# Performance work log

Hardware: AMD Instinct MI355X
Metric: run time of the kernel (lower is better)

## Reference

```python
import jax, jax.numpy as jnp
import numpy as np


def setup_inputs() -> dict:
    key = jax.random.key(0)
    k0, k1, k2 = jax.random.split(key, 3)
    B, C, N, M = 2, 64, 1024, 32
    C_mid = 16  # bottleneck of the AFA weight-learning MLP (C -> C//4 -> C)
    feature = jax.random.normal(k0, (B, C, N, M), dtype=jnp.float32)
    W1 = (jax.random.normal(k1, (C_mid, C), dtype=jnp.float32) / np.float32(np.sqrt(C)))
    b1 = jnp.zeros((C_mid,), dtype=jnp.float32)
    W2 = (jax.random.normal(k2, (C, C_mid), dtype=jnp.float32) / np.float32(np.sqrt(C_mid)))
    b2 = jnp.zeros((C,), dtype=jnp.float32)
    return {"feature": feature, "W1": W1, "b1": b1, "W2": W2, "b2": b2}


def reference(feature, W1, b1, W2, b2):
    # feature: (B, C, N, M)
    B, C, N, M = feature.shape
    eye = jnp.eye(M, dtype=feature.dtype)  # (M, M)
    # pair[b,c,n,i,j] = f_i - f_j + f_i * delta_ij  (the repeat/transpose/eye trick)
    fi = feature[..., :, None]                      # (B, C, N, M, 1)
    pair = fi - feature[..., None, :] + fi * eye    # (B, C, N, M, M)
    # 1x1-conv MLP over channel dim (SharedMLP: C -> C_mid -> C), ReLU between
    h = jax.nn.relu(jnp.einsum('oc,bcnij->bonij', W1, pair)
                    + b1[None, :, None, None, None])
    w = (jnp.einsum('oc,bcnij->bonij', W2, h)
         + b2[None, :, None, None, None])           # (B, C, N, M, M)
    w = jax.nn.softmax(w, axis=-1)                  # use_softmax=True, over last dim
    # weighted-sum aggregation over j -> (B, C, N, M)
    return jnp.sum(pair * w, axis=-1)
```

## Files before the change

### kernel.cpp

```cpp
#include <hip/hip_runtime.h>
#include <stdint.h>

namespace {
constexpr int NM = 1024 * 32;

typedef _Float16 half8 __attribute__((ext_vector_type(8)));
typedef float floatx16 __attribute__((ext_vector_type(16)));

__global__ __launch_bounds__(256, 3) void afa_kernel(
    const float* __restrict__ feat,
    const float* __restrict__ W1,
    const float* __restrict__ b1,
    const float* __restrict__ W2,
    float* __restrict__ out)
{
  __shared__ __align__(16) float f_c[64 * 34];
  __shared__ __align__(16) float g1T[16 * 33];
  __shared__ __align__(16) float w1s[16 * 68];
  __shared__ __align__(16) float edia[64 * 34];
  __shared__ __align__(16) float outs[64 * 34];

  const int t = threadIdx.x;
  const int bn = blockIdx.x;
  const size_t base = (size_t)(bn >> 10) * (64 * NM) + (size_t)(bn & 1023) * 32;

  {
    const int o = t >> 4, cq = t & 15;
    reinterpret_cast<float4*>(w1s)[o * 17 + cq] =
        reinterpret_cast<const float4*>(W1)[t];
  }
  {
    const int m = t & 31, c0 = t >> 5;
    #pragma unroll
    for (int r = 0; r < 8; ++r) {
      const int c = c0 + 8 * r;
      f_c[c * 34 + m] = feat[base + (size_t)c * NM + m];
    }
  }
  __syncthreads();

  {
    const int m = t & 31;
    const int o2 = t >> 5;
    const float* wa = w1s + o2 * 68;
    const float* wb = w1s + (o2 + 8) * 68;
    float a0 = 0.f, a1 = 0.f;
    #pragma unroll
    for (int c = 0; c < 64; ++c) {
      const float v = f_c[c * 34 + m];
      a0 = fmaf(wa[c], v, a0);
      a1 = fmaf(wb[c], v, a1);
    }
    g1T[o2 * 33 + m] = a0;
    g1T[(o2 + 8) * 33 + m] = a1;
  }
  __syncthreads();

  const int w  = t >> 6;
  const int ln = t & 63;
  const int cl = ln & 31;
  const int hl = ln >> 5;

  half8 B0, B1;
  {
    const float4* w2a = reinterpret_cast<const float4*>(W2 + cl * 16 + 8 * hl);
    const float4 x = w2a[0], y = w2a[1];
    B0[0] = (_Float16)x.x; B0[1] = (_Float16)x.y; B0[2] = (_Float16)x.z; B0[3] = (_Float16)x.w;
    B0[4] = (_Float16)y.x; B0[5] = (_Float16)y.y; B0[6] = (_Float16)y.z; B0[7] = (_Float16)y.w;
    const float4* w2b = reinterpret_cast<const float4*>(W2 + (cl + 32) * 16 + 8 * hl);
    const float4 u = w2b[0], v = w2b[1];
    B1[0] = (_Float16)u.x; B1[1] = (_Float16)u.y; B1[2] = (_Float16)u.z; B1[3] = (_Float16)u.w;
    B1[4] = (_Float16)v.x; B1[5] = (_Float16)v.y; B1[6] = (_Float16)v.z; B1[7] = (_Float16)v.w;
  }
  float b1r[8];
  {
    const float4* bb = reinterpret_cast<const float4*>(b1 + 8 * hl);
    const float4 x = bb[0], y = bb[1];
    b1r[0] = x.x; b1r[1] = x.y; b1r[2] = x.z; b1r[3] = x.w;
    b1r[4] = y.x; b1r[5] = y.y; b1r[6] = y.z; b1r[7] = y.w;
  }
  float g1j[8];
  #pragma unroll
  for (int q = 0; q < 8; ++q) g1j[q] = g1T[(8 * hl + q) * 33 + cl];

  float fcol0[16], fcol1[16];
  #pragma unroll
  for (int r = 0; r < 16; ++r) {
    const int jr = (r & 3) + 8 * (r >> 2) + 4 * hl;
    fcol0[r] = f_c[cl * 34 + jr];
    fcol1[r] = f_c[(cl + 32) * 34 + jr];
  }

  if (w == 0) {
    half8 Ad;
    #pragma unroll
    for (int q = 0; q < 8; ++q) Ad[q] = (_Float16)fmaxf(g1j[q] + b1r[q], 0.f);
    floatx16 d0, d1;
    #pragma unroll
    for (int r = 0; r < 16; ++r) { d0[r] = 0.f; d1[r] = 0.f; }
    d0 = __builtin_amdgcn_mfma_f32_32x32x16_f16(Ad, B0, d0, 0, 0, 0);
    d1 = __builtin_amdgcn_mfma_f32_32x32x16_f16(Ad, B1, d1, 0, 0, 0);
    #pragma unroll
    for (int r = 0; r < 16; ++r) {
      const int ir = (r & 3) + 8 * (r >> 2) + 4 * hl;
      edia[cl * 34 + ir]        = __expf(d0[r]);
      edia[(cl + 32) * 34 + ir] = __expf(d1[r]);
    }
  }
  __syncthreads();

  #pragma unroll 2
  for (int ii = 0; ii < 8; ++ii) {
    const int i = w * 8 + ii;
    half8 A;
    const bool dg = (cl == i);
    #pragma unroll
    for (int q = 0; q < 8; ++q) {
      const float gp = g1T[(8 * hl + q) * 33 + i] + b1r[q];
      const float h = gp - (dg ? 0.f : g1j[q]);
      A[q] = (_Float16)fmaxf(h, 0.f);
    }
    floatx16 acc0, acc1;
    #pragma unroll
    for (int r = 0; r < 16; ++r) { acc0[r] = 0.f; acc1[r] = 0.f; }
    acc0 = __builtin_amdgcn_mfma_f32_32x32x16_f16(A, B0, acc0, 0, 0, 0);
    acc1 = __builtin_amdgcn_mfma_f32_32x32x16_f16(A, B1, acc1, 0, 0, 0);

    float Sa = 0.f, Sb = 0.f, Da = 0.f, Db = 0.f;
    float Sc = 0.f, Sd = 0.f, Dc = 0.f, Dd = 0.f;
    #pragma unroll
    for (int r = 0; r < 16; r += 2) {
      const float e0 = __expf(acc0[r]);
      const float e1 = __expf(acc0[r + 1]);
      Sa += e0; Sb += e1;
      Da = fmaf(fcol0[r], e0, Da);
      Db = fmaf(fcol0[r + 1], e1, Db);
      const float e2 = __expf(acc1[r]);
      const float e3 = __expf(acc1[r + 1]);
      Sc += e2; Sd += e3;
      Dc = fmaf(fcol1[r], e2, Dc);
      Dd = fmaf(fcol1[r + 1], e3, Dd);
    }
    float S0 = Sa + Sb, D0 = Da + Db;
    float S1 = Sc + Sd, D1 = Dc + Dd;
    S0 += __shfl_xor(S0, 32);
    D0 += __shfl_xor(D0, 32);
    S1 += __shfl_xor(S1, 32);
    D1 += __shfl_xor(D1, 32);

    const float fi0 = f_c[cl * 34 + i];
    const float ei0 = edia[cl * 34 + i];
    const float fi1 = f_c[(cl + 32) * 34 + i];
    const float ei1 = edia[(cl + 32) * 34 + i];
    const float inv0 = 1.0f / S0;
    const float inv1 = 1.0f / S1;
    outs[cl * 34 + i]        = fi0 * (1.0f + ei0 * inv0) - D0 * inv0;
    outs[(cl + 32) * 34 + i] = fi1 * (1.0f + ei1 * inv1) - D1 * inv1;
  }
  __syncthreads();

  {
    const int m = t & 31, c0 = t >> 5;
    #pragma unroll
    for (int r = 0; r < 8; ++r) {
      const int cc = c0 + 8 * r;
      out[base + (size_t)cc * NM + m] = outs[cc * 34 + m];
    }
  }
}
}

extern "C" void kernel_launch(void* const* d_in, const int* in_sizes, int n_in,
                              void* d_out, int out_size, void* d_ws, size_t ws_size,
                              hipStream_t stream) {
  const float* feat = (const float*)d_in[0];
  const float* W1   = (const float*)d_in[1];
  const float* b1   = (const float*)d_in[2];
  const float* W2   = (const float*)d_in[3];
  float* out = (float*)d_out;

  afa_kernel<<<dim3(2 * 1024), dim3(256), 0, stream>>>(feat, W1, b1, W2, out);
}
```

Baseline: 38.85 us.

## Fold log2e into W2, use exp2 and packed math, cut LDS and raise occupancy

Pre-scales W2 by log2(e) so the softmax exponentials become native exp2 calls. The first-layer bias is folded into the g1 accumulation, and g1 is stored row-major so each i row can be read with float4 loads. fp16 conversion uses packed cvt_pkrtz, and the S/D reductions use 2-wide vectors. The output buffer is aliased onto edia, which removes one LDS array and lets launch bounds target 6 blocks per CU. The risks are register spills under the tighter bound and small numeric changes from round-toward-zero conversion.

```diff
diff --git a/kernel.cpp b/kernel.cpp
--- a/kernel.cpp
+++ b/kernel.cpp
@@ -3,11 +3,20 @@
 
 namespace {
 constexpr int NM = 1024 * 32;
+constexpr float LOG2E = 1.44269504088896340736f;
 
 typedef _Float16 half8 __attribute__((ext_vector_type(8)));
 typedef float floatx16 __attribute__((ext_vector_type(16)));
-
-__global__ __launch_bounds__(256, 3) void afa_kernel(
+typedef float f2v __attribute__((ext_vector_type(2)));
+
+__device__ __forceinline__ uint32_t pkrtz_bits(float a, float b) {
+  auto pk = __builtin_amdgcn_cvt_pkrtz(a, b);
+  uint32_t u;
+  __builtin_memcpy(&u, &pk, 4);
+  return u;
+}
+
+__global__ __launch_bounds__(256, 6) void afa_kernel(
     const float* __restrict__ feat,
     const float* __restrict__ W1,
     const float* __restrict__ b1,
@@ -15,15 +24,44 @@
     float* __restrict__ out)
 {
   __shared__ __align__(16) float f_c[64 * 34];
-  __shared__ __align__(16) float g1T[16 * 33];
+  __shared__ __align__(16) float g1b[32 * 20];
   __shared__ __align__(16) float w1s[16 * 68];
   __shared__ __align__(16) float edia[64 * 34];
-  __shared__ __align__(16) float outs[64 * 34];
 
   const int t = threadIdx.x;
   const int bn = blockIdx.x;
   const size_t base = (size_t)(bn >> 10) * (64 * NM) + (size_t)(bn & 1023) * 32;
 
+  const int w  = t >> 6;
+  const int ln = t & 63;
+  const int cl = ln & 31;
+  const int hl = ln >> 5;
+
+  half8 B0, B1;
+  {
+    const float4* w2a = reinterpret_cast<const float4*>(W2 + cl * 16 + 8 * hl);
+    const float4 x = w2a[0], y = w2a[1];
+    B0[0] = (_Float16)(x.x * LOG2E); B0[1] = (_Float16)(x.y * LOG2E);
+    B0[2] = (_Float16)(x.z * LOG2E); B0[3] = (_Float16)(x.w * LOG2E);
+    B0[4] = (_Float16)(y.x * LOG2E); B0[5] = (_Float16)(y.y * LOG2E);
+    B0[6] = (_Float16)(y.z * LOG2E); B0[7] = (_Float16)(y.w * LOG2E);
+    const float4* w2b = reinterpret_cast<const float4*>(W2 + (cl + 32) * 16 + 8 * hl);
+    const float4 u = w2b[0], v = w2b[1];
+    B1[0] = (_Float16)(u.x * LOG2E); B1[1] = (_Float16)(u.y * LOG2E);
+    B1[2] = (_Float16)(u.z * LOG2E); B1[3] = (_Float16)(u.w * LOG2E);
+    B1[4] = (_Float16)(v.x * LOG2E); B1[5] = (_Float16)(v.y * LOG2E);
+    B1[6] = (_Float16)(v.z * LOG2E); B1[7] = (_Float16)(v.w * LOG2E);
+  }
+  float b1r[8];
+  {
+    const float4* bb = reinterpret_cast<const float4*>(b1 + 8 * hl);
+    const float4 x = bb[0], y = bb[1];
+    b1r[0] = x.x; b1r[1] = x.y; b1r[2] = x.z; b1r[3] = x.w;
+    b1r[4] = y.x; b1r[5] = y.y; b1r[6] = y.z; b1r[7] = y.w;
+  }
+  const float b1a = b1[t >> 5];
+  const float b1b = b1[(t >> 5) + 8];
+
   {
     const int o = t >> 4, cq = t & 15;
     reinterpret_cast<float4*>(w1s)[o * 17 + cq] =
@@ -40,48 +78,19 @@
   __syncthreads();
 
   {
-    const int m = t & 31;
-    const int o2 = t >> 5;
+    const int m = t & 31, o2 = t >> 5;
     const float* wa = w1s + o2 * 68;
     const float* wb = w1s + (o2 + 8) * 68;
-    float a0 = 0.f, a1 = 0.f;
+    float a0 = b1a, a1 = b1b;
     #pragma unroll
     for (int c = 0; c < 64; ++c) {
       const float v = f_c[c * 34 + m];
       a0 = fmaf(wa[c], v, a0);
       a1 = fmaf(wb[c], v, a1);
     }
-    g1T[o2 * 33 + m] = a0;
-    g1T[(o2 + 8) * 33 + m] = a1;
-  }
-  __syncthreads();
-
-  const int w  = t >> 6;
-  const int ln = t & 63;
-  const int cl = ln & 31;
-  const int hl = ln >> 5;
-
-  half8 B0, B1;
-  {
-    const float4* w2a = reinterpret_cast<const float4*>(W2 + cl * 16 + 8 * hl);
-    const float4 x = w2a[0], y = w2a[1];
-    B0[0] = (_Float16)x.x; B0[1] = (_Float16)x.y; B0[2] = (_Float16)x.z; B0[3] = (_Float16)x.w;
-    B0[4] = (_Float16)y.x; B0[5] = (_Float16)y.y; B0[6] = (_Float16)y.z; B0[7] = (_Float16)y.w;
-    const float4* w2b = reinterpret_cast<const float4*>(W2 + (cl + 32) * 16 + 8 * hl);
-    const float4 u = w2b[0], v = w2b[1];
-    B1[0] = (_Float16)u.x; B1[1] = (_Float16)u.y; B1[2] = (_Float16)u.z; B1[3] = (_Float16)u.w;
-    B1[4] = (_Float16)v.x; B1[5] = (_Float16)v.y; B1[6] = (_Float16)v.z; B1[7] = (_Float16)v.w;
-  }
-  float b1r[8];
-  {
-    const float4* bb = reinterpret_cast<const float4*>(b1 + 8 * hl);
-    const float4 x = bb[0], y = bb[1];
-    b1r[0] = x.x; b1r[1] = x.y; b1r[2] = x.z; b1r[3] = x.w;
-    b1r[4] = y.x; b1r[5] = y.y; b1r[6] = y.z; b1r[7] = y.w;
-  }
-  float g1j[8];
-  #pragma unroll
-  for (int q = 0; q < 8; ++q) g1j[q] = g1T[(8 * hl + q) * 33 + cl];
+    g1b[m * 20 + o2] = a0;
+    g1b[m * 20 + o2 + 8] = a1;
+  }
 
   float fcol0[16], fcol1[16];
   #pragma unroll
@@ -90,21 +99,34 @@
     fcol0[r] = f_c[cl * 34 + jr];
     fcol1[r] = f_c[(cl + 32) * 34 + jr];
   }
+  __syncthreads();
+
+  float gj[8], gjn[8];
+  {
+    const float4* gp = reinterpret_cast<const float4*>(g1b + cl * 20 + 8 * hl);
+    const float4 x = gp[0], y = gp[1];
+    gj[0] = x.x; gj[1] = x.y; gj[2] = x.z; gj[3] = x.w;
+    gj[4] = y.x; gj[5] = y.y; gj[6] = y.z; gj[7] = y.w;
+  }
+  #pragma unroll
+  for (int q = 0; q < 8; ++q) gjn[q] = b1r[q] - gj[q];
 
   if (w == 0) {
-    half8 Ad;
-    #pragma unroll
-    for (int q = 0; q < 8; ++q) Ad[q] = (_Float16)fmaxf(g1j[q] + b1r[q], 0.f);
+    union { half8 h; uint32_t u[4]; } au;
+    #pragma unroll
+    for (int p = 0; p < 4; ++p) {
+      au.u[p] = pkrtz_bits(fmaxf(gj[2 * p], 0.f), fmaxf(gj[2 * p + 1], 0.f));
+    }
     floatx16 d0, d1;
     #pragma unroll
     for (int r = 0; r < 16; ++r) { d0[r] = 0.f; d1[r] = 0.f; }
-    d0 = __builtin_amdgcn_mfma_f32_32x32x16_f16(Ad, B0, d0, 0, 0, 0);
-    d1 = __builtin_amdgcn_mfma_f32_32x32x16_f16(Ad, B1, d1, 0, 0, 0);
+    d0 = __builtin_amdgcn_mfma_f32_32x32x16_f16(au.h, B0, d0, 0, 0, 0);
+    d1 = __builtin_amdgcn_mfma_f32_32x32x16_f16(au.h, B1, d1, 0, 0, 0);
     #pragma unroll
     for (int r = 0; r < 16; ++r) {
       const int ir = (r & 3) + 8 * (r >> 2) + 4 * hl;
-      edia[cl * 34 + ir]        = __expf(d0[r]);
-      edia[(cl + 32) * 34 + ir] = __expf(d1[r]);
+      edia[cl * 34 + ir]        = __builtin_amdgcn_exp2f(d0[r]);
+      edia[(cl + 32) * 34 + ir] = __builtin_amdgcn_exp2f(d1[r]);
     }
   }
   __syncthreads();
@@ -112,50 +134,50 @@
   #pragma unroll 2
   for (int ii = 0; ii < 8; ++ii) {
     const int i = w * 8 + ii;
-    half8 A;
     const bool dg = (cl == i);
-    #pragma unroll
-    for (int q = 0; q < 8; ++q) {
-      const float gp = g1T[(8 * hl + q) * 33 + i] + b1r[q];
-      const float h = gp - (dg ? 0.f : g1j[q]);
-      A[q] = (_Float16)fmaxf(h, 0.f);
+    const float4* gi4 = reinterpret_cast<const float4*>(g1b + i * 20 + 8 * hl);
+    const float4 gx = gi4[0], gy = gi4[1];
+    const float gi[8] = {gx.x, gx.y, gx.z, gx.w, gy.x, gy.y, gy.z, gy.w};
+    union { half8 h; uint32_t u[4]; } au;
+    #pragma unroll
+    for (int p = 0; p < 4; ++p) {
+      const float h0 = fmaxf(gi[2 * p]     + (dg ? 0.f : gjn[2 * p]),     0.f);
+      const float h1 = fmaxf(gi[2 * p + 1] + (dg ? 0.f : gjn[2 * p + 1]), 0.f);
+      au.u[p] = pkrtz_bits(h0, h1);
     }
     floatx16 acc0, acc1;
     #pragma unroll
     for (int r = 0; r < 16; ++r) { acc0[r] = 0.f; acc1[r] = 0.f; }
-    acc0 = __builtin_amdgcn_mfma_f32_32x32x16_f16(A, B0, acc0, 0, 0, 0);
-    acc1 = __builtin_amdgcn_mfma_f32_32x32x16_f16(A, B1, acc1, 0, 0, 0);
-
-    float Sa = 0.f, Sb = 0.f, Da = 0.f, Db = 0.f;
-    float Sc = 0.f, Sd = 0.f, Dc = 0.f, Dd = 0.f;
+    acc0 = __builtin_amdgcn_mfma_f32_32x32x16_f16(au.h, B0, acc0, 0, 0, 0);
+    acc1 = __builtin_amdgcn_mfma_f32_32x32x16_f16(au.h, B1, acc1, 0, 0, 0);
+
+    f2v S0 = {0.f, 0.f}, D0 = {0.f, 0.f}, S1 = {0.f, 0.f}, D1 = {0.f, 0.f};
     #pragma unroll
     for (int r = 0; r < 16; r += 2) {
-      const float e0 = __expf(acc0[r]);
-      const float e1 = __expf(acc0[r + 1]);
-      Sa += e0; Sb += e1;
-      Da = fmaf(fcol0[r], e0, Da);
-      Db = fmaf(fcol0[r + 1], e1, Db);
-      const float e2 = __expf(acc1[r]);
-      const float e3 = __expf(acc1[r + 1]);
-      Sc += e2; Sd += e3;
-      Dc = fmaf(fcol1[r], e2, Dc);
-      Dd = fmaf(fcol1[r + 1], e3, Dd);
-    }
-    float S0 = Sa + Sb, D0 = Da + Db;
-    float S1 = Sc + Sd, D1 = Dc + Dd;
-    S0 += __shfl_xor(S0, 32);
-    D0 += __shfl_xor(D0, 32);
-    S1 += __shfl_xor(S1, 32);
-    D1 += __shfl_xor(D1, 32);
+      const f2v e0 = {__builtin_amdgcn_exp2f(acc0[r]),
+                      __builtin_amdgcn_exp2f(acc0[r + 1])};
+      const f2v fc0 = {fcol0[r], fcol0[r + 1]};
+      S0 += e0;
+      D0 += fc0 * e0;
+      const f2v e1 = {__builtin_amdgcn_exp2f(acc1[r]),
+                      __builtin_amdgcn_exp2f(acc1[r + 1])};
+      const f2v fc1 = {fcol1[r], fcol1[r + 1]};
+      S1 += e1;
+      D1 += fc1 * e1;
+    }
+    float Sa = S0.x + S0.y, Da = D0.x + D0.y;
+    float Sb = S1.x + S1.y, Db = D1.x + D1.y;
+    Sa += __shfl_xor(Sa, 32); Da += __shfl_xor(Da, 32);
+    Sb += __shfl_xor(Sb, 32); Db += __shfl_xor(Db, 32);
 
     const float fi0 = f_c[cl * 34 + i];
     const float ei0 = edia[cl * 34 + i];
     const float fi1 = f_c[(cl + 32) * 34 + i];
     const float ei1 = edia[(cl + 32) * 34 + i];
-    const float inv0 = 1.0f / S0;
-    const float inv1 = 1.0f / S1;
-    outs[cl * 34 + i]        = fi0 * (1.0f + ei0 * inv0) - D0 * inv0;
-    outs[(cl + 32) * 34 + i] = fi1 * (1.0f + ei1 * inv1) - D1 * inv1;
+    const float inv0 = 1.0f / Sa;
+    const float inv1 = 1.0f / Sb;
+    edia[cl * 34 + i]        = fi0 * (1.0f + ei0 * inv0) - Da * inv0;
+    edia[(cl + 32) * 34 + i] = fi1 * (1.0f + ei1 * inv1) - Db * inv1;
   }
   __syncthreads();
 
@@ -164,7 +186,7 @@
     #pragma unroll
     for (int r = 0; r < 8; ++r) {
       const int cc = c0 + 8 * r;
-      out[base + (size_t)cc * NM + m] = outs[cc * 34 + m];
+      out[base + (size_t)cc * NM + m] = edia[cc * 34 + m];
     }
   }
 }
```

After: 64.24 us. 1.65x slower.
